# Kernel optimization log

Hardware: AMD Instinct MI355X
Metric: run time of the kernel (lower is better)

Reference implementation:

```python
import jax, jax.numpy as jnp
import numpy as np

N = 50000
E = 800000
IN_CH = 128
HID = 32
HEADS = 4
OUT_CH = 2
NEG_SLOPE = 0.2


def setup_inputs() -> dict:
    key = jax.random.key(0)
    ks = jax.random.split(key, 10)
    x = jax.random.normal(ks[0], (N, IN_CH), dtype=jnp.float32)
    edge_index = jax.random.randint(ks[1], (2, E), 0, N, dtype=jnp.int32)
    s1 = 1.0 / np.sqrt(IN_CH)
    s2 = 1.0 / np.sqrt(HEADS * HID)
    return {
        "x": x,
        "edge_index": edge_index,
        "W1": jax.random.normal(ks[2], (IN_CH, HEADS * HID), dtype=jnp.float32) * s1,
        "a_src1": jax.random.normal(ks[3], (HEADS, HID), dtype=jnp.float32) * s2,
        "a_dst1": jax.random.normal(ks[4], (HEADS, HID), dtype=jnp.float32) * s2,
        "b1": jnp.zeros((HEADS * HID,), dtype=jnp.float32),
        "W2": jax.random.normal(ks[5], (HEADS * HID, 1 * OUT_CH), dtype=jnp.float32) * s2,
        "a_src2": jax.random.normal(ks[6], (1, OUT_CH), dtype=jnp.float32),
        "a_dst2": jax.random.normal(ks[7], (1, OUT_CH), dtype=jnp.float32),
        "b2": jnp.zeros((OUT_CH,), dtype=jnp.float32),
    }


def gat_layer(x, edge_index, W, a_src, a_dst, bias, heads, out_ch, concat):
    # PyG GATConv: linear -> per-node attn terms -> per-edge LeakyReLU ->
    # softmax over incoming edges (self-loops added) -> scatter-add aggregate.
    n = x.shape[0]
    loop = jnp.arange(n, dtype=edge_index.dtype)
    src = jnp.concatenate([edge_index[0], loop])  # [E+N]
    dst = jnp.concatenate([edge_index[1], loop])
    h = (x @ W).reshape(n, heads, out_ch)                 # [N, H, C]
    a_s = jnp.einsum('nhc,hc->nh', h, a_src)              # [N, H]
    a_d = jnp.einsum('nhc,hc->nh', h, a_dst)
    e = jax.nn.leaky_relu(a_s[src] + a_d[dst], NEG_SLOPE)  # [E+N, H]
    m = jax.ops.segment_max(e, dst, num_segments=n)
    m = jax.lax.stop_gradient(jnp.where(jnp.isfinite(m), m, 0.0))
    p = jnp.exp(e - m[dst])
    denom = jax.ops.segment_sum(p, dst, num_segments=n)
    alpha = p / (denom[dst] + 1e-16)                       # softmax per dst node
    msg = h[src] * alpha[:, :, None]                       # [E+N, H, C]
    out = jax.ops.segment_sum(msg, dst, num_segments=n)    # [N, H, C]
    out = out.reshape(n, heads * out_ch) if concat else out.mean(axis=1)
    return out + bias


def reference(x, edge_index, W1, a_src1, a_dst1, b1, W2, a_src2, a_dst2, b2):
    h = gat_layer(x, edge_index, W1, a_src1, a_dst1, b1, HEADS, HID, True)
    h = jax.nn.relu(h)  # dropout is identity in eval mode
    o = gat_layer(h, edge_index, W2, a_src2, a_dst2, b2, 1, OUT_CH, False)
    return jax.nn.log_softmax(o, axis=1)
```

## Files before the change

### kernel.cpp

```cpp
#include <hip/hip_runtime.h>
#include <hip/hip_bf16.h>

#define NEG_SLOPE 0.2f
#define INV_LN2 1.44269504088896340736f
#define BSH   6
#define BUKSZ 64
#define MAXBUK 1024
#define CHUNK 2048
#define XPAD  136

typedef __attribute__((ext_vector_type(8))) short bf16x8;
typedef __attribute__((ext_vector_type(4))) float f32x4;

__device__ __forceinline__ float exp2lrelu(float z) {
    return __builtin_amdgcn_exp2f(fmaxf(z, NEG_SLOPE * z));
}

__device__ __forceinline__ unsigned short f2bf(float f) {
    unsigned int u = __float_as_uint(f);
    u = (u + 0x7fffu + ((u >> 16) & 1u)) >> 16;
    return (unsigned short)u;
}

__device__ __forceinline__ float2 bfpair(unsigned int u) {
    float2 r;
    r.x = __uint_as_float(u << 16);
    r.y = __uint_as_float(u & 0xffff0000u);
    return r;
}

__global__ __launch_bounds__(256) void k0_prep(const float* __restrict__ W1,
                                               const float* __restrict__ a_src1,
                                               const float* __restrict__ a_dst1,
                                               unsigned short* __restrict__ w1t,
                                               int* __restrict__ bcnt,
                                               int* __restrict__ gcur, int nbuk) {
    int g = blockIdx.x * 256 + threadIdx.x;
    if (g < nbuk) { bcnt[g] = 0; gcur[g] = 0; }
    if (g < 128 * 128) {
        int k = g >> 7, nn = g & 127;
        w1t[nn * 128 + k] = f2bf(W1[g]);
    } else if (g < 128 * 128 + 1024) {
        int e = g - 128 * 128;
        int row8 = e >> 7;
        int k = e & 127;
        int h = row8 & 3;
        const float* av = (row8 < 4) ? a_src1 : a_dst1;
        float s = 0.f;
#pragma unroll
        for (int c = 0; c < 32; ++c)
            s += W1[k * 128 + h * 32 + c] * av[h * 32 + c];
        w1t[(128 + row8) * 128 + k] = f2bf(s * INV_LN2);
    } else if (g < 128 * 128 + 2048) {
        int e = g - (128 * 128 + 1024);
        w1t[(136 + (e >> 7)) * 128 + (e & 127)] = 0;
    }
}

__global__ __launch_bounds__(256) void k1_fat(const float* __restrict__ x,
                                              const unsigned short* __restrict__ w1t,
                                              unsigned short* __restrict__ h1b,
                                              float* __restrict__ a_s1,
                                              float* __restrict__ a_d1, int n,
                                              const int* __restrict__ e_dst, int e,
                                              int nbuk, int nblk,
                                              int* __restrict__ bcnt) {
    __shared__ unsigned short xsh[64 * XPAD];
    __shared__ unsigned short wsh[144 * XPAD];
    const int tid = threadIdx.x;

    if (blockIdx.x < (unsigned)nblk) {
        int* lcnt = (int*)xsh;
        const int bid = blockIdx.x;
        for (int b = tid; b < nbuk; b += 256) lcnt[b] = 0;
        __syncthreads();
        const int e0 = bid * CHUNK;
        const int e1 = min(e, e0 + CHUNK);
        for (int k = e0 + tid; k < e1; k += 256)
            atomicAdd(&lcnt[e_dst[k] >> BSH], 1);
        __syncthreads();
        for (int b = tid; b < nbuk; b += 256) {
            int c = lcnt[b];
            if (c) atomicAdd(&bcnt[b], c);
        }
        return;
    }

    const int row0 = (blockIdx.x - nblk) * 64;
    {
        const bf16x8* w1v = (const bf16x8*)w1t;
#pragma unroll
        for (int ii = 0; ii < 9; ++ii) {
            int i = tid + ii * 256;
            int r = i >> 4, c = (i & 15) * 8;
            *(bf16x8*)&wsh[r * XPAD + c] = w1v[i];
        }
    }
#pragma unroll
    for (int i = 0; i < 8; ++i) {
        int idx = tid + i * 256;
        int r = idx >> 5;
        int c = (idx & 31) * 4;
        int gr = row0 + r;
        float4 v = make_float4(0.f, 0.f, 0.f, 0.f);
        if (gr < n) v = *(const float4*)&x[(size_t)gr * 128 + c];
        ushort4 b;
        b.x = f2bf(v.x); b.y = f2bf(v.y); b.z = f2bf(v.z); b.w = f2bf(v.w);
        *(ushort4*)&xsh[r * XPAD + c] = b;
    }
    __syncthreads();

    const int wave = tid >> 6;
    const int lane = tid & 63;
    const int quad = lane >> 4;
    const int l16 = lane & 15;

    bf16x8 afrag[4];
#pragma unroll
    for (int ks = 0; ks < 4; ++ks)
        afrag[ks] = *(const bf16x8*)&xsh[(wave * 16 + l16) * XPAD + ks * 32 + quad * 8];

    f32x4 acc[9];
#pragma unroll
    for (int t = 0; t < 9; ++t) acc[t] = (f32x4){0.f, 0.f, 0.f, 0.f};

#pragma unroll
    for (int t = 0; t < 9; ++t) {
#pragma unroll
        for (int ks = 0; ks < 4; ++ks) {
            bf16x8 bfrag = *(const bf16x8*)&wsh[(t * 16 + l16) * XPAD + ks * 32 + quad * 8];
            acc[t] = __builtin_amdgcn_mfma_f32_16x16x32_bf16(afrag[ks], bfrag, acc[t], 0, 0, 0);
        }
    }

#pragma unroll
    for (int r = 0; r < 4; ++r) {
        int gr = row0 + wave * 16 + quad * 4 + r;
        if (gr < n) {
            if (l16 < 4)      a_s1[gr * 4 + l16]       = acc[8][r];
            else if (l16 < 8) a_d1[gr * 4 + (l16 - 4)] = acc[8][r];
        }
    }

    __syncthreads();
#pragma unroll
    for (int t = 0; t < 8; ++t)
#pragma unroll
        for (int r = 0; r < 4; ++r)
            xsh[(wave * 16 + quad * 4 + r) * XPAD + t * 16 + l16] = f2bf(acc[t][r]);
    __syncthreads();
#pragma unroll
    for (int i = 0; i < 8; ++i) {
        int idx = tid + i * 256;
        int r = idx >> 5;
        int c = (idx & 31) * 4;
        int gr = row0 + r;
        if (gr < n)
            *(ushort4*)&h1b[(size_t)gr * 128 + c] = *(ushort4*)&xsh[r * XPAD + c];
    }
}

__global__ __launch_bounds__(256) void kb_place3(const int* __restrict__ src,
                                                 const int* __restrict__ dst, int e,
                                                 int nbuk, const int* __restrict__ bcnt,
                                                 int* __restrict__ gcur,
                                                 unsigned int* __restrict__ part,
                                                 int* __restrict__ bbase) {
    __shared__ int lbase[MAXBUK];
    __shared__ int lcur[MAXBUK];
    __shared__ int s[256];
    const int tid = threadIdx.x;
    const int bid = blockIdx.x;
    int t4 = tid * 4;
    int v0 = (t4     < nbuk) ? bcnt[t4]     : 0;
    int v1 = (t4 + 1 < nbuk) ? bcnt[t4 + 1] : 0;
    int v2 = (t4 + 2 < nbuk) ? bcnt[t4 + 2] : 0;
    int v3 = (t4 + 3 < nbuk) ? bcnt[t4 + 3] : 0;
    int ssum = v0 + v1 + v2 + v3;
    s[tid] = ssum;
    for (int b = tid; b < nbuk; b += 256) lcur[b] = 0;
    __syncthreads();
    for (int off = 1; off < 256; off <<= 1) {
        int t = (tid >= off) ? s[tid - off] : 0;
        __syncthreads();
        s[tid] += t;
        __syncthreads();
    }
    int excl = s[tid] - ssum;
    if (t4 < nbuk)     lbase[t4]     = excl;
    if (t4 + 1 < nbuk) lbase[t4 + 1] = excl + v0;
    if (t4 + 2 < nbuk) lbase[t4 + 2] = excl + v0 + v1;
    if (t4 + 3 < nbuk) lbase[t4 + 3] = excl + v0 + v1 + v2;
    __syncthreads();
    if (bid == 0) {
        for (int b = tid; b < nbuk; b += 256) bbase[b] = lbase[b];
        if (tid == 255) bbase[nbuk] = s[255];
    }
    const int e0 = bid * CHUNK;
    const int e1 = min(e, e0 + CHUNK);
    for (int k = e0 + tid; k < e1; k += 256)
        atomicAdd(&lcur[dst[k] >> BSH], 1);
    __syncthreads();
    for (int b = tid; b < nbuk; b += 256) {
        int c = lcur[b];
        if (c) lcur[b] = lbase[b] + atomicAdd(&gcur[b], c);
    }
    __syncthreads();
    for (int k = e0 + tid; k < e1; k += 256) {
        int d = dst[k];
        int pos = atomicAdd(&lcur[d >> BSH], 1);
        part[pos] = ((unsigned int)src[k] << 16) | (unsigned int)(d & 0xffff);
    }
}

__global__ __launch_bounds__(256) void kc_csr(const unsigned int* __restrict__ part,
                                              const int* __restrict__ bbase, int nbuk,
                                              int* __restrict__ row_start,
                                              unsigned short* __restrict__ csr_src) {
    __shared__ int cnt[64];
    __shared__ int cur[64];
    const int b = blockIdx.x;
    const int tid = threadIdx.x;
    const int eb = bbase[b];
    const int nE = bbase[b + 1] - eb;
    if (tid < 64) cnt[tid] = 0;
    __syncthreads();
    for (int k = tid; k < nE; k += 256)
        atomicAdd(&cnt[part[eb + k] & 63u], 1);
    __syncthreads();
    if (tid < 64) {
        int v = cnt[tid];
        int incl = v;
#pragma unroll
        for (int off = 1; off < 64; off <<= 1) {
            int t = __shfl_up(incl, off);
            if (tid >= off) incl += t;
        }
        int excl = incl - v;
        cur[tid] = excl;
        row_start[(b << BSH) + tid] = eb + excl;
        if (tid == 63 && b == nbuk - 1) row_start[(b << BSH) + 64] = eb + incl;
    }
    __syncthreads();
    for (int k = tid; k < nE; k += 256) {
        unsigned int u = part[eb + k];
        int pos = atomicAdd(&cur[u & 63u], 1);
        csr_src[eb + pos] = (unsigned short)(u >> 16);
    }
}

__global__ __launch_bounds__(256) void k3_agg1(
    const unsigned short* __restrict__ h1b, const float* __restrict__ a_s1,
    const float* __restrict__ a_d1, const int* __restrict__ row_start,
    const unsigned short* __restrict__ csr_src, const float* __restrict__ b1,
    const float* __restrict__ W2, const float* __restrict__ a_src2,
    const float* __restrict__ a_dst2, float4* __restrict__ pk, int n) {
    const int wid = (blockIdx.x * blockDim.x + threadIdx.x) >> 6;
    const int lane = threadIdx.x & 63;
    if (wid >= n) return;
    const int q = lane >> 4;
    const int l16 = lane & 15;
    const int c0 = l16 * 8;
    const unsigned cb = (unsigned)l16 * 16u;
    const int head = l16 >> 2;
    const int rs = row_start[wid];
    const int deg = row_start[wid + 1] - rs;
    const float ad = a_d1[wid * 4 + head];
    const char* __restrict__ h1c = (const char*)h1b;
    const unsigned short* __restrict__ crs = csr_src + rs;

    float dnm = 0.f;
    float acc[8] = {};
    const int dm1 = deg - 1;
    const int rounded = (deg + 15) & ~15;
    uint4 g0 = make_uint4(0, 0, 0, 0), g1 = g0, g2 = g0, g3 = g0;
    for (int j = q; j < rounded; j += 16) {
        int i0 = min(j,      dm1);
        int i1 = min(j + 4,  dm1);
        int i2 = min(j + 8,  dm1);
        int i3 = min(j + 12, dm1);
        unsigned s0 = (unsigned)crs[i0];
        unsigned s1 = (unsigned)crs[i1];
        unsigned s2 = (unsigned)crs[i2];
        unsigned s3 = (unsigned)crs[i3];
        float as0 = a_s1[(s0 << 2) + head];
        float as1 = a_s1[(s1 << 2) + head];
        float as2 = a_s1[(s2 << 2) + head];
        float as3 = a_s1[(s3 << 2) + head];
        const bool b0 = j      < deg;
        const bool b1 = j + 4  < deg;
        const bool b2 = j + 8  < deg;
        const bool b3 = j + 12 < deg;
        if (b0) g0 = *(const uint4*)(h1c + ((s0 << 8) + cb));
        if (b1) g1 = *(const uint4*)(h1c + ((s1 << 8) + cb));
        if (b2) g2 = *(const uint4*)(h1c + ((s2 << 8) + cb));
        if (b3) g3 = *(const uint4*)(h1c + ((s3 << 8) + cb));
        float p0 = b0 ? exp2lrelu(as0 + ad) : 0.f;
        float p1 = b1 ? exp2lrelu(as1 + ad) : 0.f;
        float p2 = b2 ? exp2lrelu(as2 + ad) : 0.f;
        float p3 = b3 ? exp2lrelu(as3 + ad) : 0.f;
        dnm += (p0 + p1) + (p2 + p3);
        float2 v0a = bfpair(g0.x), v0b = bfpair(g0.y), v0c = bfpair(g0.z), v0d = bfpair(g0.w);
        float2 v1a = bfpair(g1.x), v1b = bfpair(g1.y), v1c = bfpair(g1.z), v1d = bfpair(g1.w);
        float2 v2a = bfpair(g2.x), v2b = bfpair(g2.y), v2c = bfpair(g2.z), v2d = bfpair(g2.w);
        float2 v3a = bfpair(g3.x), v3b = bfpair(g3.y), v3c = bfpair(g3.z), v3d = bfpair(g3.w);
        acc[0] += (p0 * v0a.x + p1 * v1a.x) + (p2 * v2a.x + p3 * v3a.x);
        acc[1] += (p0 * v0a.y + p1 * v1a.y) + (p2 * v2a.y + p3 * v3a.y);
        acc[2] += (p0 * v0b.x + p1 * v1b.x) + (p2 * v2b.x + p3 * v3b.x);
        acc[3] += (p0 * v0b.y + p1 * v1b.y) + (p2 * v2b.y + p3 * v3b.y);
        acc[4] += (p0 * v0c.x + p1 * v1c.x) + (p2 * v2c.x + p3 * v3c.x);
        acc[5] += (p0 * v0c.y + p1 * v1c.y) + (p2 * v2c.y + p3 * v3c.y);
        acc[6] += (p0 * v0d.x + p1 * v1d.x) + (p2 * v2d.x + p3 * v3d.x);
        acc[7] += (p0 * v0d.y + p1 * v1d.y) + (p2 * v2d.y + p3 * v3d.y);
    }
    dnm += __shfl_xor(dnm, 16);
    dnm += __shfl_xor(dnm, 32);
#pragma unroll
    for (int k = 0; k < 8; ++k) {
        acc[k] += __shfl_xor(acc[k], 16);
        acc[k] += __shfl_xor(acc[k], 32);
    }
    {
        float p = exp2lrelu(a_s1[wid * 4 + head] + ad);
        uint4 gs = *(const uint4*)(h1c + (((unsigned)wid << 8) + cb));
        float2 ha = bfpair(gs.x), hb = bfpair(gs.y), hc = bfpair(gs.z), hd2 = bfpair(gs.w);
        dnm += p;
        acc[0] += p * ha.x;  acc[1] += p * ha.y;
        acc[2] += p * hb.x;  acc[3] += p * hb.y;
        acc[4] += p * hc.x;  acc[5] += p * hc.y;
        acc[6] += p * hd2.x; acc[7] += p * hd2.y;
    }
    float inv = 1.f / (dnm + 1e-16f);
    float r[8];
    float4 bva = *(const float4*)&b1[c0];
    float4 bvb = *(const float4*)&b1[c0 + 4];
    r[0] = fmaxf(acc[0] * inv + bva.x, 0.f);
    r[1] = fmaxf(acc[1] * inv + bva.y, 0.f);
    r[2] = fmaxf(acc[2] * inv + bva.z, 0.f);
    r[3] = fmaxf(acc[3] * inv + bva.w, 0.f);
    r[4] = fmaxf(acc[4] * inv + bvb.x, 0.f);
    r[5] = fmaxf(acc[5] * inv + bvb.y, 0.f);
    r[6] = fmaxf(acc[6] * inv + bvb.z, 0.f);
    r[7] = fmaxf(acc[7] * inv + bvb.w, 0.f);

    float p0 = 0.f, p1 = 0.f;
#pragma unroll
    for (int k = 0; k < 4; ++k) {
        float4 w = *(const float4*)&W2[c0 * 2 + k * 4];
        p0 += r[2 * k] * w.x + r[2 * k + 1] * w.z;
        p1 += r[2 * k] * w.y + r[2 * k + 1] * w.w;
    }
#pragma unroll
    for (int off = 1; off < 16; off <<= 1) {
        p0 += __shfl_xor(p0, off);
        p1 += __shfl_xor(p1, off);
    }
    if (lane == 0) {
        pk[wid] = make_float4(p0, p1,
                              (p0 * a_src2[0] + p1 * a_src2[1]) * INV_LN2,
                              (p0 * a_dst2[0] + p1 * a_dst2[1]) * INV_LN2);
    }
}

__global__ __launch_bounds__(256) void k4_agg2(
    const float4* __restrict__ pk, const int* __restrict__ row_start,
    const unsigned short* __restrict__ csr_src, const float* __restrict__ b2,
    float* __restrict__ out, int n) {
    const int g = blockIdx.x * blockDim.x + threadIdx.x;
    const int lane = threadIdx.x & 63;
    const int node = (g >> 6) * 4 + (lane >> 4);
    const int l16 = lane & 15;
    if (node >= n) return;
    const int rs = row_start[node];
    const int deg = row_start[node + 1] - rs;
    const float4 me = pk[node];
    const float ad = me.w;

    float dnm = 0.f, a0 = 0.f, a1 = 0.f;
    for (int j = l16; j < deg; j += 16) {
        int s = (int)csr_src[rs + j];
        float4 qv = pk[s];
        float p = exp2lrelu(qv.z + ad);
        dnm += p;
        a0 += p * qv.x;
        a1 += p * qv.y;
    }
    if (l16 == 0) {
        float p = exp2lrelu(me.z + ad);
        dnm += p;
        a0 += p * me.x;
        a1 += p * me.y;
    }
#pragma unroll
    for (int off = 1; off < 16; off <<= 1) {
        dnm += __shfl_xor(dnm, off);
        a0 += __shfl_xor(a0, off);
        a1 += __shfl_xor(a1, off);
    }
    if (l16 == 0) {
        float inv = 1.f / (dnm + 1e-16f);
        float o0 = a0 * inv + b2[0];
        float o1 = a1 * inv + b2[1];
        float m2 = fmaxf(o0, o1);
        float lse = m2 + logf(__expf(o0 - m2) + __expf(o1 - m2));
        out[node * 2 + 0] = o0 - lse;
        out[node * 2 + 1] = o1 - lse;
    }
}

extern "C" void kernel_launch(void* const* d_in, const int* in_sizes, int n_in,
                              void* d_out, int out_size, void* d_ws, size_t ws_size,
                              hipStream_t stream) {
    const float* x      = (const float*)d_in[0];
    const int*   ei     = (const int*)d_in[1];
    const float* W1     = (const float*)d_in[2];
    const float* a_src1 = (const float*)d_in[3];
    const float* a_dst1 = (const float*)d_in[4];
    const float* b1     = (const float*)d_in[5];
    const float* W2     = (const float*)d_in[6];
    const float* a_src2 = (const float*)d_in[7];
    const float* a_dst2 = (const float*)d_in[8];
    const float* b2     = (const float*)d_in[9];
    float* out = (float*)d_out;

    const int N = in_sizes[0] / 128;
    const int E = in_sizes[1] / 2;
    const int* e_src = ei;
    const int* e_dst = ei + E;

    const int NBUK = (N + BUKSZ - 1) >> BSH;
    const int nblk = (E + CHUNK - 1) / CHUNK;
    const int gemmBlocks = (N + 63) / 64;

    char* p = (char*)d_ws;
    auto alloc = [&](size_t bytes) -> void* {
        void* r = (void*)p;
        p += (bytes + 255) & ~(size_t)255;
        return r;
    };
    unsigned short* h1b   = (unsigned short*)alloc((size_t)N * 128 * 2);
    float*          a_s1  = (float*)alloc((size_t)N * 4 * 4);
    float*          a_d1  = (float*)alloc((size_t)N * 4 * 4);
    float4*         pk    = (float4*)alloc((size_t)N * 16);
    unsigned short* w1t   = (unsigned short*)alloc((size_t)144 * 128 * 2);
    int*            bcnt  = (int*)alloc((size_t)NBUK * 4);
    int*            gcur  = (int*)alloc((size_t)NBUK * 4);
    int*            bbase = (int*)alloc((size_t)(NBUK + 1) * 4);
    unsigned int*   part  = (unsigned int*)alloc((size_t)E * 4);
    int*            row_start = (int*)alloc(((size_t)NBUK * BUKSZ + 1) * 4);
    unsigned short* csr_src   = (unsigned short*)alloc((size_t)E * 2);

    k0_prep<<<72, 256, 0, stream>>>(W1, a_src1, a_dst1, w1t, bcnt, gcur, NBUK);
    k1_fat<<<nblk + gemmBlocks, 256, 0, stream>>>(x, w1t, h1b, a_s1, a_d1, N,
                                                  e_dst, E, NBUK, nblk, bcnt);
    kb_place3<<<nblk, 256, 0, stream>>>(e_src, e_dst, E, NBUK, bcnt, gcur, part, bbase);
    kc_csr<<<NBUK, 256, 0, stream>>>(part, bbase, NBUK, row_start, csr_src);

    k3_agg1<<<(N * 64 + 255) / 256, 256, 0, stream>>>(h1b, a_s1, a_d1, row_start, csr_src,
                                                      b1, W2, a_src2, a_dst2, pk, N);
    k4_agg2<<<((N + 3) / 4 * 64 + 255) / 256, 256, 0, stream>>>(pk, row_start, csr_src,
                                                                b2, out, N);
}
```

Before: 177.9 us.

## Fuse CSR construction into histogram kernel with in-kernel subset barriers

```diff
diff --git a/kernel.cpp b/kernel.cpp
--- a/kernel.cpp
+++ b/kernel.cpp
@@ -29,14 +29,30 @@
     return r;
 }
 
+__device__ __forceinline__ void subset_barrier(int* ctr, int target) {
+    __syncthreads();
+    if (threadIdx.x == 0) {
+        __threadfence();
+        atomicAdd(ctr, 1);
+        while (__hip_atomic_load(ctr, __ATOMIC_ACQUIRE,
+                                 __HIP_MEMORY_SCOPE_AGENT) < target)
+            __builtin_amdgcn_s_sleep(8);
+    }
+    __syncthreads();
+}
+
 __global__ __launch_bounds__(256) void k0_prep(const float* __restrict__ W1,
                                                const float* __restrict__ a_src1,
                                                const float* __restrict__ a_dst1,
                                                unsigned short* __restrict__ w1t,
+                                               int* __restrict__ ncnt,
                                                int* __restrict__ bcnt,
-                                               int* __restrict__ gcur, int nbuk) {
+                                               int* __restrict__ sync,
+                                               int nbuk, int n) {
     int g = blockIdx.x * 256 + threadIdx.x;
-    if (g < nbuk) { bcnt[g] = 0; gcur[g] = 0; }
+    if (g < n) ncnt[g] = 0;
+    if (g < nbuk) bcnt[g] = 0;
+    if (g < 2) sync[g] = 0;
     if (g < 128 * 128) {
         int k = g >> 7, nn = g & 127;
         w1t[nn * 128 + k] = f2bf(W1[g]);
@@ -57,31 +73,83 @@
     }
 }
 
-__global__ __launch_bounds__(256) void k1_fat(const float* __restrict__ x,
-                                              const unsigned short* __restrict__ w1t,
-                                              unsigned short* __restrict__ h1b,
-                                              float* __restrict__ a_s1,
-                                              float* __restrict__ a_d1, int n,
-                                              const int* __restrict__ e_dst, int e,
-                                              int nbuk, int nblk,
-                                              int* __restrict__ bcnt) {
+__global__ __launch_bounds__(256, 2) void k1_fat(
+    const float* __restrict__ x, const unsigned short* __restrict__ w1t,
+    unsigned short* __restrict__ h1b, float* __restrict__ a_s1,
+    float* __restrict__ a_d1, int n, const int* __restrict__ e_src,
+    const int* __restrict__ e_dst, int e, int nbuk, int nblk,
+    int* __restrict__ bcnt, int* __restrict__ ncnt, int* __restrict__ ncur,
+    int* __restrict__ row_start, unsigned short* __restrict__ csr_src,
+    int* __restrict__ sync) {
     __shared__ unsigned short xsh[64 * XPAD];
     __shared__ unsigned short wsh[144 * XPAD];
     const int tid = threadIdx.x;
 
     if (blockIdx.x < (unsigned)nblk) {
-        int* lcnt = (int*)xsh;
+        int* lcnt  = (int*)xsh;
+        int* lbase = (int*)wsh;
+        int* s     = (int*)wsh + MAXBUK;
         const int bid = blockIdx.x;
         for (int b = tid; b < nbuk; b += 256) lcnt[b] = 0;
         __syncthreads();
         const int e0 = bid * CHUNK;
         const int e1 = min(e, e0 + CHUNK);
-        for (int k = e0 + tid; k < e1; k += 256)
-            atomicAdd(&lcnt[e_dst[k] >> BSH], 1);
+        for (int k = e0 + tid; k < e1; k += 256) {
+            int d = e_dst[k];
+            atomicAdd(&lcnt[d >> BSH], 1);
+            atomicAdd(&ncnt[d], 1);
+        }
         __syncthreads();
         for (int b = tid; b < nbuk; b += 256) {
             int c = lcnt[b];
             if (c) atomicAdd(&bcnt[b], c);
+        }
+        subset_barrier(&sync[0], nblk);
+        int t4 = tid * 4;
+        int v0 = (t4     < nbuk) ? bcnt[t4]     : 0;
+        int v1 = (t4 + 1 < nbuk) ? bcnt[t4 + 1] : 0;
+        int v2 = (t4 + 2 < nbuk) ? bcnt[t4 + 2] : 0;
+        int v3 = (t4 + 3 < nbuk) ? bcnt[t4 + 3] : 0;
+        int ssum = v0 + v1 + v2 + v3;
+        s[tid] = ssum;
+        __syncthreads();
+        for (int off = 1; off < 256; off <<= 1) {
+            int t = (tid >= off) ? s[tid - off] : 0;
+            __syncthreads();
+            s[tid] += t;
+            __syncthreads();
+        }
+        int excl = s[tid] - ssum;
+        if (t4 < nbuk)     lbase[t4]     = excl;
+        if (t4 + 1 < nbuk) lbase[t4 + 1] = excl + v0;
+        if (t4 + 2 < nbuk) lbase[t4 + 2] = excl + v0 + v1;
+        if (t4 + 3 < nbuk) lbase[t4 + 3] = excl + v0 + v1 + v2;
+        __syncthreads();
+        const int wv = tid >> 6, lane = tid & 63;
+        if (wv < 2) {
+            for (int bb = 2 * bid + wv; bb < nbuk; bb += 2 * nblk) {
+                int node = (bb << BSH) + lane;
+                int v = (node < n) ? ncnt[node] : 0;
+                int incl = v;
+#pragma unroll
+                for (int off = 1; off < 64; off <<= 1) {
+                    int t = __shfl_up(incl, off);
+                    if (lane >= off) incl += t;
+                }
+                int base = lbase[bb];
+                if (node < n) {
+                    int r0 = base + incl - v;
+                    row_start[node] = r0;
+                    ncur[node] = r0;
+                }
+                if (bb == nbuk - 1 && lane == 63) row_start[n] = base + incl;
+            }
+        }
+        subset_barrier(&sync[1], nblk);
+        for (int k = e0 + tid; k < e1; k += 256) {
+            int d = e_dst[k];
+            int pos = atomicAdd(&ncur[d], 1);
+            csr_src[pos] = (unsigned short)e_src[k];
         }
         return;
     }
@@ -157,95 +225,6 @@
         int gr = row0 + r;
         if (gr < n)
             *(ushort4*)&h1b[(size_t)gr * 128 + c] = *(ushort4*)&xsh[r * XPAD + c];
-    }
-}
-
-__global__ __launch_bounds__(256) void kb_place3(const int* __restrict__ src,
-                                                 const int* __restrict__ dst, int e,
-                                                 int nbuk, const int* __restrict__ bcnt,
-                                                 int* __restrict__ gcur,
-                                                 unsigned int* __restrict__ part,
-                                                 int* __restrict__ bbase) {
-    __shared__ int lbase[MAXBUK];
-    __shared__ int lcur[MAXBUK];
-    __shared__ int s[256];
-    const int tid = threadIdx.x;
-    const int bid = blockIdx.x;
-    int t4 = tid * 4;
-    int v0 = (t4     < nbuk) ? bcnt[t4]     : 0;
-    int v1 = (t4 + 1 < nbuk) ? bcnt[t4 + 1] : 0;
-    int v2 = (t4 + 2 < nbuk) ? bcnt[t4 + 2] : 0;
-    int v3 = (t4 + 3 < nbuk) ? bcnt[t4 + 3] : 0;
-    int ssum = v0 + v1 + v2 + v3;
-    s[tid] = ssum;
-    for (int b = tid; b < nbuk; b += 256) lcur[b] = 0;
-    __syncthreads();
-    for (int off = 1; off < 256; off <<= 1) {
-        int t = (tid >= off) ? s[tid - off] : 0;
-        __syncthreads();
-        s[tid] += t;
-        __syncthreads();
-    }
-    int excl = s[tid] - ssum;
-    if (t4 < nbuk)     lbase[t4]     = excl;
-    if (t4 + 1 < nbuk) lbase[t4 + 1] = excl + v0;
-    if (t4 + 2 < nbuk) lbase[t4 + 2] = excl + v0 + v1;
-    if (t4 + 3 < nbuk) lbase[t4 + 3] = excl + v0 + v1 + v2;
-    __syncthreads();
-    if (bid == 0) {
-        for (int b = tid; b < nbuk; b += 256) bbase[b] = lbase[b];
-        if (tid == 255) bbase[nbuk] = s[255];
-    }
-    const int e0 = bid * CHUNK;
-    const int e1 = min(e, e0 + CHUNK);
-    for (int k = e0 + tid; k < e1; k += 256)
-        atomicAdd(&lcur[dst[k] >> BSH], 1);
-    __syncthreads();
-    for (int b = tid; b < nbuk; b += 256) {
-        int c = lcur[b];
-        if (c) lcur[b] = lbase[b] + atomicAdd(&gcur[b], c);
-    }
-    __syncthreads();
-    for (int k = e0 + tid; k < e1; k += 256) {
-        int d = dst[k];
-        int pos = atomicAdd(&lcur[d >> BSH], 1);
-        part[pos] = ((unsigned int)src[k] << 16) | (unsigned int)(d & 0xffff);
-    }
-}
-
-__global__ __launch_bounds__(256) void kc_csr(const unsigned int* __restrict__ part,
-                                              const int* __restrict__ bbase, int nbuk,
-                                              int* __restrict__ row_start,
-                                              unsigned short* __restrict__ csr_src) {
-    __shared__ int cnt[64];
-    __shared__ int cur[64];
-    const int b = blockIdx.x;
-    const int tid = threadIdx.x;
-    const int eb = bbase[b];
-    const int nE = bbase[b + 1] - eb;
-    if (tid < 64) cnt[tid] = 0;
-    __syncthreads();
-    for (int k = tid; k < nE; k += 256)
-        atomicAdd(&cnt[part[eb + k] & 63u], 1);
-    __syncthreads();
-    if (tid < 64) {
-        int v = cnt[tid];
-        int incl = v;
-#pragma unroll
-        for (int off = 1; off < 64; off <<= 1) {
-            int t = __shfl_up(incl, off);
-            if (tid >= off) incl += t;
-        }
-        int excl = incl - v;
-        cur[tid] = excl;
-        row_start[(b << BSH) + tid] = eb + excl;
-        if (tid == 63 && b == nbuk - 1) row_start[(b << BSH) + 64] = eb + incl;
-    }
-    __syncthreads();
-    for (int k = tid; k < nE; k += 256) {
-        unsigned int u = part[eb + k];
-        int pos = atomicAdd(&cur[u & 63u], 1);
-        csr_src[eb + pos] = (unsigned short)(u >> 16);
     }
 }
 
@@ -271,10 +250,41 @@
 
     float dnm = 0.f;
     float acc[8] = {};
-    const int dm1 = deg - 1;
-    const int rounded = (deg + 15) & ~15;
-    uint4 g0 = make_uint4(0, 0, 0, 0), g1 = g0, g2 = g0, g3 = g0;
-    for (int j = q; j < rounded; j += 16) {
+    const int nfull = deg >> 4;
+    int j = q;
+    for (int it = 0; it < nfull; ++it, j += 16) {
+        unsigned s0 = (unsigned)crs[j];
+        unsigned s1 = (unsigned)crs[j + 4];
+        unsigned s2 = (unsigned)crs[j + 8];
+        unsigned s3 = (unsigned)crs[j + 12];
+        float as0 = a_s1[(s0 << 2) + head];
+        float as1 = a_s1[(s1 << 2) + head];
+        float as2 = a_s1[(s2 << 2) + head];
+        float as3 = a_s1[(s3 << 2) + head];
+        uint4 g0 = *(const uint4*)(h1c + ((s0 << 8) + cb));
+        uint4 g1 = *(const uint4*)(h1c + ((s1 << 8) + cb));
+        uint4 g2 = *(const uint4*)(h1c + ((s2 << 8) + cb));
+        uint4 g3 = *(const uint4*)(h1c + ((s3 << 8) + cb));
+        float p0 = exp2lrelu(as0 + ad);
+        float p1 = exp2lrelu(as1 + ad);
+        float p2 = exp2lrelu(as2 + ad);
+        float p3 = exp2lrelu(as3 + ad);
+        dnm += (p0 + p1) + (p2 + p3);
+        float2 v0a = bfpair(g0.x), v0b = bfpair(g0.y), v0c = bfpair(g0.z), v0d = bfpair(g0.w);
+        float2 v1a = bfpair(g1.x), v1b = bfpair(g1.y), v1c = bfpair(g1.z), v1d = bfpair(g1.w);
+        float2 v2a = bfpair(g2.x), v2b = bfpair(g2.y), v2c = bfpair(g2.z), v2d = bfpair(g2.w);
+        float2 v3a = bfpair(g3.x), v3b = bfpair(g3.y), v3c = bfpair(g3.z), v3d = bfpair(g3.w);
+        acc[0] += (p0 * v0a.x + p1 * v1a.x) + (p2 * v2a.x + p3 * v3a.x);
+        acc[1] += (p0 * v0a.y + p1 * v1a.y) + (p2 * v2a.y + p3 * v3a.y);
+        acc[2] += (p0 * v0b.x + p1 * v1b.x) + (p2 * v2b.x + p3 * v3b.x);
+        acc[3] += (p0 * v0b.y + p1 * v1b.y) + (p2 * v2b.y + p3 * v3b.y);
+        acc[4] += (p0 * v0c.x + p1 * v1c.x) + (p2 * v2c.x + p3 * v3c.x);
+        acc[5] += (p0 * v0c.y + p1 * v1c.y) + (p2 * v2c.y + p3 * v3c.y);
+        acc[6] += (p0 * v0d.x + p1 * v1d.x) + (p2 * v2d.x + p3 * v3d.x);
+        acc[7] += (p0 * v0d.y + p1 * v1d.y) + (p2 * v2d.y + p3 * v3d.y);
+    }
+    if (deg & 15) {
+        const int dm1 = deg - 1;
         int i0 = min(j,      dm1);
         int i1 = min(j + 4,  dm1);
         int i2 = min(j + 8,  dm1);
@@ -291,6 +301,7 @@
         const bool b1 = j + 4  < deg;
         const bool b2 = j + 8  < deg;
         const bool b3 = j + 12 < deg;
+        uint4 g0 = make_uint4(0, 0, 0, 0), g1 = g0, g2 = g0, g3 = g0;
         if (b0) g0 = *(const uint4*)(h1c + ((s0 << 8) + cb));
         if (b1) g1 = *(const uint4*)(h1c + ((s1 << 8) + cb));
         if (b2) g2 = *(const uint4*)(h1c + ((s2 << 8) + cb));
@@ -444,18 +455,18 @@
     float4*         pk    = (float4*)alloc((size_t)N * 16);
     unsigned short* w1t   = (unsigned short*)alloc((size_t)144 * 128 * 2);
     int*            bcnt  = (int*)alloc((size_t)NBUK * 4);
-    int*            gcur  = (int*)alloc((size_t)NBUK * 4);
-    int*            bbase = (int*)alloc((size_t)(NBUK + 1) * 4);
-    unsigned int*   part  = (unsigned int*)alloc((size_t)E * 4);
-    int*            row_start = (int*)alloc(((size_t)NBUK * BUKSZ + 1) * 4);
+    int*            ncnt  = (int*)alloc((size_t)N * 4);
+    int*            ncur  = (int*)alloc((size_t)N * 4);
+    int*            row_start = (int*)alloc(((size_t)N + 64) * 4);
     unsigned short* csr_src   = (unsigned short*)alloc((size_t)E * 2);
-
-    k0_prep<<<72, 256, 0, stream>>>(W1, a_src1, a_dst1, w1t, bcnt, gcur, NBUK);
+    int*            sync  = (int*)alloc(256);
+
+    k0_prep<<<(N + 255) / 256, 256, 0, stream>>>(W1, a_src1, a_dst1, w1t,
+                                                 ncnt, bcnt, sync, NBUK, N);
     k1_fat<<<nblk + gemmBlocks, 256, 0, stream>>>(x, w1t, h1b, a_s1, a_d1, N,
-                                                  e_dst, E, NBUK, nblk, bcnt);
-    kb_place3<<<nblk, 256, 0, stream>>>(e_src, e_dst, E, NBUK, bcnt, gcur, part, bbase);
-    kc_csr<<<NBUK, 256, 0, stream>>>(part, bbase, NBUK, row_start, csr_src);
-
+                                                  e_src, e_dst, E, NBUK, nblk,
+                                                  bcnt, ncnt, ncur, row_start,
+                                                  csr_src, sync);
     k3_agg1<<<(N * 64 + 255) / 256, 256, 0, stream>>>(h1b, a_s1, a_d1, row_start, csr_src,
                                                       b1, W2, a_src2, a_dst2, pk, N);
     k4_agg2<<<((N + 3) / 4 * 64 + 255) / 256, 256, 0, stream>>>(pk, row_start, csr_src,
```

Result: slower. 303.9 us (+70.8%).
